# Kernel tuning notes

Hardware: AMD Instinct MI355X
Metric: run time of the kernel (lower is better)

## Reference

```python
import jax, jax.numpy as jnp
import numpy as np

HEADS = 8
DIM_HEAD = 64
IMG_SIZE = 32
KERNEL = 5
DILATION = 1
SEQ_LEN = 1280
IMG_SEQ_LEN = IMG_SIZE * IMG_SIZE  # 1024
TEXT_LEN = SEQ_LEN - IMG_SEQ_LEN   # 256


def _unfold(t, k, pad, dil, pad_value=0.0):
    # t: (b, c, H, W) -> (b, c, H*W, k*k), matching torch F.unfold ordering (c major)
    b, c, H, W = t.shape
    tp = jnp.pad(t, ((0, 0), (0, 0), (pad, pad), (pad, pad)), constant_values=pad_value)
    off = jnp.arange(k) * dil
    ys = jnp.arange(H)[:, None] + off[None, :]  # (H, k)
    xs = jnp.arange(W)[:, None] + off[None, :]  # (W, k)
    p = tp[:, :, ys[:, None, :, None], xs[None, :, None, :]]  # (b, c, H, W, k, k)
    return p.reshape(b, c, H * W, k * k)


def setup_inputs() -> dict:
    key = jax.random.key(0)
    k0, k1, k2 = jax.random.split(key, 3)
    b, n, dim = 4, SEQ_LEN, 512
    inner = HEADS * DIM_HEAD
    x = jax.random.normal(k0, (b, n, dim), dtype=jnp.float32)
    mask = jnp.ones((b, TEXT_LEN), dtype=bool)
    W_qkv = jax.random.normal(k1, (dim, 3 * inner), dtype=jnp.float32) * 0.02
    W_out = jax.random.normal(k2, (inner, dim), dtype=jnp.float32) * 0.02
    b_out = jnp.zeros((dim,), dtype=jnp.float32)
    return {"x": x, "mask": mask, "W_qkv": W_qkv, "W_out": W_out, "b_out": b_out}


def reference(x, mask, W_qkv, W_out, b_out):
    # t2i branch of SparseConvCausalAttention.forward
    b, n, dim = x.shape
    h, d = HEADS, DIM_HEAD
    scale = d ** -0.5
    neg = -jnp.finfo(x.dtype).max
    eff_k = (KERNEL - 1) * DILATION + 1
    pad = eff_k // 2

    qkv = x @ W_qkv  # (b, n, 3*h*d); n == SEQ_LEN so F.pad is a no-op
    qkv = qkv.reshape(b, n, 3, h, d).transpose(2, 0, 3, 1, 4).reshape(3, b * h, n, d)
    q, k, v = qkv[0] * scale, qkv[1], qkv[2]

    q_text, q_img = q[:, :TEXT_LEN], q[:, TEXT_LEN:]
    k_text, k_img = k[:, :TEXT_LEN], k[:, TEXT_LEN:]
    v_text, v_img = v[:, :TEXT_LEN], v[:, TEXT_LEN:]

    # --- text -> text causal attention ---
    dots_text = jnp.einsum('bid,bjd->bij', q_text, k_text)  # (bh, T, T)
    causal_t = jnp.triu(jnp.ones((TEXT_LEN, TEXT_LEN), bool), 1)
    pad_mask = jnp.repeat(mask, h, axis=0)[:, None, :]  # (bh, 1, T)
    dots_text = jnp.where(causal_t[None], neg, dots_text)
    dots_text = jnp.where(~pad_mask, neg, dots_text)
    attn_text = jax.nn.softmax(dots_text, axis=-1)
    out_text = jnp.einsum('bij,bjd->bid', attn_text, v_text)

    # --- image local-window (unfold) keys/values ---
    k_im = k_img.transpose(0, 2, 1).reshape(b * h, d, IMG_SIZE, IMG_SIZE)
    v_im = v_img.transpose(0, 2, 1).reshape(b * h, d, IMG_SIZE, IMG_SIZE)
    kk = KERNEL * KERNEL
    k_patch = _unfold(k_im, KERNEL, pad, DILATION).transpose(0, 2, 3, 1)  # (bh, I, kk, d)
    v_patch = _unfold(v_im, KERNEL, pad, DILATION).transpose(0, 2, 3, 1)

    dots_image = jnp.einsum('bid,bijd->bij', q_img, k_patch)       # (bh, I, kk)
    dots_i2t = jnp.einsum('bid,bjd->bij', q_img, k_text)           # (bh, I, T)

    # local causal mask via unfolded position indices (out-of-bounds -> IMG_SEQ_LEN)
    idx_img = jnp.arange(IMG_SEQ_LEN, dtype=jnp.float32).reshape(1, 1, IMG_SIZE, IMG_SIZE)
    k_idx = _unfold(idx_img, KERNEL, pad, DILATION, pad_value=float(IMG_SEQ_LEN))
    k_idx = k_idx.reshape(IMG_SEQ_LEN, kk)  # (I, kk)
    q_idx = jnp.arange(IMG_SEQ_LEN, dtype=jnp.float32)[:, None]
    causal_img = q_idx < k_idx  # (I, kk)

    full_mask = jnp.concatenate(
        (jnp.broadcast_to(~pad_mask, (b * h, IMG_SEQ_LEN, TEXT_LEN)),
         jnp.broadcast_to(causal_img[None], (b * h, IMG_SEQ_LEN, kk))), axis=-1)
    dots = jnp.concatenate((dots_i2t, dots_image), axis=-1)
    dots = jnp.where(full_mask, neg, dots)
    attn = jax.nn.softmax(dots, axis=-1)
    attn_i2t, attn_ii = attn[..., :TEXT_LEN], attn[..., TEXT_LEN:]

    out_img = (jnp.einsum('bij,bijd->bid', attn_ii, v_patch)
               + jnp.einsum('bij,bjd->bid', attn_i2t, v_text))

    out = jnp.concatenate((out_text, out_img), axis=1)  # (bh, n, d)
    out = out.reshape(b, h, n, d).transpose(0, 2, 1, 3).reshape(b, n, h * d)
    out = out @ W_out + b_out
    return out[:, :n]
```

## Files before the change

### kernel.cpp

```cpp
#include <hip/hip_runtime.h>
#include <math.h>

#define BATCH   4
#define NSEQ    1280
#define DIM     512
#define HEADS   8
#define DHEAD   64
#define TEXTLEN 256
#define IMGLEN  1024
#define BH      (BATCH*HEADS)

typedef __bf16 bf16x8 __attribute__((ext_vector_type(8)));
typedef float  f32x4  __attribute__((ext_vector_type(4)));
typedef unsigned short u16x4 __attribute__((ext_vector_type(4)));
typedef unsigned short u16x8 __attribute__((ext_vector_type(8)));

__device__ __forceinline__ unsigned short f2bf(float f) {
  unsigned int u = __float_as_uint(f);
  u += 0x7FFFu + ((u >> 16) & 1u);
  return (unsigned short)(u >> 16);
}

template<int MODE>
__global__ __launch_bounds__(256)
void mfma_gemm(const unsigned short* __restrict__ A,
               const unsigned short* __restrict__ BT,
               unsigned short* __restrict__ qb, unsigned short* __restrict__ kb,
               unsigned short* __restrict__ vb, unsigned short* __restrict__ vt,
               float* __restrict__ outb, const float* __restrict__ bias) {
  __shared__ __align__(16) unsigned short As[128*64];
  __shared__ __align__(16) unsigned short Bs[128*64];
  const int tid  = threadIdx.x;
  const int lane = tid & 63, w = tid >> 6;
  const int wm = w >> 1, wn = w & 1;
  const int lr = lane & 15, lg = lane >> 4;
  const int bx = blockIdx.x, by = blockIdx.y;

  f32x4 acc[4][4] = {};

  for (int kt = 0; kt < 512; kt += 64) {
    __syncthreads();
#pragma unroll
    for (int u = 0; u < 4; ++u) {
      const int idx = tid + u*256;
      const int row = idx >> 3, pq = idx & 7;
      const int sc  = ((pq ^ (row & 7)) << 3);
      const unsigned short* ga = A  + (size_t)(by*128 + row)*512 + kt + sc;
      const unsigned short* gb = BT + (size_t)(bx*128 + row)*512 + kt + sc;
      unsigned short* la = As + (((u << 8) + (w << 6)) << 3);
      unsigned short* lb = Bs + (((u << 8) + (w << 6)) << 3);
      __builtin_amdgcn_global_load_lds(
          (const __attribute__((address_space(1))) void*)ga,
          (__attribute__((address_space(3))) void*)la, 16, 0, 0);
      __builtin_amdgcn_global_load_lds(
          (const __attribute__((address_space(1))) void*)gb,
          (__attribute__((address_space(3))) void*)lb, 16, 0, 0);
    }
    __syncthreads();

#pragma unroll
    for (int kk = 0; kk < 2; ++kk) {
      bf16x8 af[4], bfr[4];
#pragma unroll
      for (int mi = 0; mi < 4; ++mi) {
        const int row = wm*64 + mi*16 + lr;
        const int q   = kk*4 + lg;
        af[mi] = *(const bf16x8*)&As[row*64 + ((q ^ (row & 7)) << 3)];
      }
#pragma unroll
      for (int ni = 0; ni < 4; ++ni) {
        const int n = wn*64 + ni*16 + lr;
        const int q = kk*4 + lg;
        bfr[ni] = *(const bf16x8*)&Bs[n*64 + ((q ^ (n & 7)) << 3)];
      }
#pragma unroll
      for (int mi = 0; mi < 4; ++mi)
#pragma unroll
        for (int ni = 0; ni < 4; ++ni)
          acc[mi][ni] = __builtin_amdgcn_mfma_f32_16x16x32_bf16(
              af[mi], bfr[ni], acc[mi][ni], 0, 0, 0);
    }
  }

  if (MODE == 0) {
    const int t  = bx >> 2, bxl = bx & 3;
    const int hh = bxl*2 + wn;
    const int bb = by / 10;
    const int nb = (by - bb*10) * 128;
    const float s = (t == 0) ? 0.125f : 1.0f;
    const size_t bh64 = (size_t)(bb*HEADS + hh);
    if (t != 2) {
      unsigned short* dst = (t == 0) ? qb : kb;
      unsigned short* base = dst + (bh64*NSEQ + nb)*DHEAD;
#pragma unroll
      for (int mi = 0; mi < 4; ++mi)
#pragma unroll
        for (int ni = 0; ni < 4; ++ni)
#pragma unroll
          for (int r = 0; r < 4; ++r) {
            const int rl = wm*64 + mi*16 + lg*4 + r;
            base[(size_t)rl*DHEAD + ni*16 + lr] = f2bf(acc[mi][ni][r] * s);
          }
    } else if (nb < 256) {
      unsigned short* vtb = vt + bh64*64*TEXTLEN;
#pragma unroll
      for (int mi = 0; mi < 4; ++mi)
#pragma unroll
        for (int ni = 0; ni < 4; ++ni)
#pragma unroll
          for (int r = 0; r < 4; ++r) {
            const int rl = wm*64 + mi*16 + lg*4 + r;
            const int d  = ni*16 + lr;
            vtb[(size_t)d*TEXTLEN + nb + rl] = f2bf(acc[mi][ni][r]);
          }
    } else {
      unsigned short* base = vb + (bh64*NSEQ + nb)*DHEAD;
#pragma unroll
      for (int mi = 0; mi < 4; ++mi)
#pragma unroll
        for (int ni = 0; ni < 4; ++ni)
#pragma unroll
          for (int r = 0; r < 4; ++r) {
            const int rl = wm*64 + mi*16 + lg*4 + r;
            base[(size_t)rl*DHEAD + ni*16 + lr] = f2bf(acc[mi][ni][r]);
          }
    }
  } else {
#pragma unroll
    for (int mi = 0; mi < 4; ++mi)
#pragma unroll
      for (int ni = 0; ni < 4; ++ni)
#pragma unroll
        for (int r = 0; r < 4; ++r) {
          const int gr = by*128 + wm*64 + mi*16 + lg*4 + r;
          const int gc = bx*128 + wn*64 + ni*16 + lr;
          outb[(size_t)gr*DIM + gc] = acc[mi][ni][r] + bias[gc];
        }
  }
}

__global__ __launch_bounds__(256)
void convert_bf16(const float* __restrict__ in, unsigned short* __restrict__ out,
                  int n) {
  const int i = (blockIdx.x*256 + threadIdx.x)*8;
  if (i < n) {
    const float4 a = *(const float4*)(in + i);
    const float4 b = *(const float4*)(in + i + 4);
    u16x8 pk;
    pk[0]=f2bf(a.x); pk[1]=f2bf(a.y); pk[2]=f2bf(a.z); pk[3]=f2bf(a.w);
    pk[4]=f2bf(b.x); pk[5]=f2bf(b.y); pk[6]=f2bf(b.z); pk[7]=f2bf(b.w);
    *(u16x8*)(out + i) = pk;
  }
}

__global__ __launch_bounds__(256)
void transpose_bf16(const float* __restrict__ in, unsigned short* __restrict__ out,
                    int K, int N) {
  __shared__ float t[64][65];
  const int k0 = blockIdx.y*64, n0 = blockIdx.x*64;
  const int tx = threadIdx.x & 15, ty = threadIdx.x >> 4;
#pragma unroll
  for (int rr = 0; rr < 4; ++rr) {
    const int k = ty + rr*16;
    const float4 v = *(const float4*)(in + (size_t)(k0 + k)*N + n0 + tx*4);
    t[k][tx*4+0] = v.x; t[k][tx*4+1] = v.y; t[k][tx*4+2] = v.z; t[k][tx*4+3] = v.w;
  }
  __syncthreads();
#pragma unroll
  for (int rr = 0; rr < 4; ++rr) {
    const int n = ty + rr*16;
    u16x4 pk;
#pragma unroll
    for (int j = 0; j < 4; ++j) pk[j] = f2bf(t[tx*4+j][n]);
    *(u16x4*)(out + (size_t)(n0 + n)*K + k0 + tx*4) = pk;
  }
}

__global__ __launch_bounds__(256)
void attn_qk(const unsigned short* __restrict__ qv,
             const unsigned short* __restrict__ kv,
             unsigned short* __restrict__ Pm, float* __restrict__ lpart) {
  __shared__ __align__(16) unsigned short As[128*64];
  __shared__ __align__(16) unsigned short Bs[128*64];
  const int tid  = threadIdx.x;
  const int lane = tid & 63, w = tid >> 6;
  const int wm = w >> 1, wn = w & 1;
  const int lr = lane & 15, lg = lane >> 4;
  const int bx = blockIdx.x, by = blockIdx.y;
  const int bh = by / 10, qt = by - bh*10;
  const bool textq = qt >= 8;
  const int qsrc  = textq ? (qt - 8)*128 : (TEXTLEN + qt*128);
  const int prow0 = qt*128;
  const int qg0   = (qt - 8)*128;

  {
    const unsigned short* ga0 = qv + ((size_t)bh*NSEQ + qsrc)*DHEAD;
    const unsigned short* gb0 = kv + ((size_t)bh*NSEQ + bx*128)*DHEAD;
#pragma unroll
    for (int u = 0; u < 4; ++u) {
      const int idx = tid + u*256;
      const int row = idx >> 3, pq = idx & 7;
      const int sc  = ((pq ^ (row & 7)) << 3);
      unsigned short* la = As + (((u << 8) + (w << 6)) << 3);
      unsigned short* lb = Bs + (((u << 8) + (w << 6)) << 3);
      __builtin_amdgcn_global_load_lds(
          (const __attribute__((address_space(1))) void*)(ga0 + (size_t)row*DHEAD + sc),
          (__attribute__((address_space(3))) void*)la, 16, 0, 0);
      __builtin_amdgcn_global_load_lds(
          (const __attribute__((address_space(1))) void*)(gb0 + (size_t)row*DHEAD + sc),
          (__attribute__((address_space(3))) void*)lb, 16, 0, 0);
    }
  }
  __syncthreads();

  f32x4 acc[4][4] = {};
#pragma unroll
  for (int kk = 0; kk < 2; ++kk) {
    bf16x8 af[4], bfr[4];
#pragma unroll
    for (int mi = 0; mi < 4; ++mi) {
      const int row = wm*64 + mi*16 + lr;
      const int q   = kk*4 + lg;
      af[mi] = *(const bf16x8*)&As[row*64 + ((q ^ (row & 7)) << 3)];
    }
#pragma unroll
    for (int ni = 0; ni < 4; ++ni) {
      const int n = wn*64 + ni*16 + lr;
      const int q = kk*4 + lg;
      bfr[ni] = *(const bf16x8*)&Bs[n*64 + ((q ^ (n & 7)) << 3)];
    }
#pragma unroll
    for (int mi = 0; mi < 4; ++mi)
#pragma unroll
      for (int ni = 0; ni < 4; ++ni)
        acc[mi][ni] = __builtin_amdgcn_mfma_f32_16x16x32_bf16(
            af[mi], bfr[ni], acc[mi][ni], 0, 0, 0);
  }

  unsigned short* pbase = Pm + ((size_t)bh*NSEQ + prow0)*TEXTLEN;
  float* lbase = lpart + ((size_t)bh*NSEQ + prow0)*4;
#pragma unroll
  for (int mi = 0; mi < 4; ++mi)
#pragma unroll
    for (int r = 0; r < 4; ++r) {
      const int q_local = wm*64 + mi*16 + lg*4 + r;
      float ps = 0.f;
#pragma unroll
      for (int ni = 0; ni < 4; ++ni) {
        const int key = bx*128 + wn*64 + ni*16 + lr;
        float wv = __expf(acc[mi][ni][r]);
        if (textq && key > qg0 + q_local) wv = 0.f;
        ps += wv;
        pbase[(size_t)q_local*TEXTLEN + key] = f2bf(wv);
      }
      ps += __shfl_xor(ps, 1);
      ps += __shfl_xor(ps, 2);
      ps += __shfl_xor(ps, 4);
      ps += __shfl_xor(ps, 8);
      if (lr == 0) lbase[(size_t)q_local*4 + bx*2 + wn] = ps;
    }
}

__global__ __launch_bounds__(256)
void attn_pv(const unsigned short* __restrict__ Pm,
             const unsigned short* __restrict__ vt,
             float* __restrict__ Of) {
  __shared__ __align__(16) unsigned short As[256*64];
  __shared__ __align__(16) unsigned short Bs[64*64];
  const int tid  = threadIdx.x;
  const int lane = tid & 63, w = tid >> 6;
  const int lr = lane & 15, lg = lane >> 4;
  const int mt = blockIdx.x, bh = blockIdx.y;

  f32x4 acc[4][4] = {};

  for (int kt = 0; kt < TEXTLEN; kt += 64) {
    __syncthreads();
    {
      const unsigned short* ga0 = Pm + ((size_t)bh*NSEQ + mt*256)*TEXTLEN + kt;
      const unsigned short* gb0 = vt + ((size_t)bh*DHEAD)*TEXTLEN + kt;
#pragma unroll
      for (int u = 0; u < 8; ++u) {
        const int idx = tid + u*256;
        const int row = idx >> 3, pq = idx & 7;
        const int sc  = ((pq ^ (row & 7)) << 3);
        unsigned short* la = As + (((u << 8) + (w << 6)) << 3);
        __builtin_amdgcn_global_load_lds(
            (const __attribute__((address_space(1))) void*)(ga0 + (size_t)row*TEXTLEN + sc),
            (__attribute__((address_space(3))) void*)la, 16, 0, 0);
      }
#pragma unroll
      for (int u = 0; u < 2; ++u) {
        const int idx = tid + u*256;
        const int row = idx >> 3, pq = idx & 7;
        const int sc  = ((pq ^ (row & 7)) << 3);
        unsigned short* lb = Bs + (((u << 8) + (w << 6)) << 3);
        __builtin_amdgcn_global_load_lds(
            (const __attribute__((address_space(1))) void*)(gb0 + (size_t)row*TEXTLEN + sc),
            (__attribute__((address_space(3))) void*)lb, 16, 0, 0);
      }
    }
    __syncthreads();

#pragma unroll
    for (int kk = 0; kk < 2; ++kk) {
      bf16x8 af[4], bfr[4];
#pragma unroll
      for (int mi = 0; mi < 4; ++mi) {
        const int row = w*64 + mi*16 + lr;
        const int q   = kk*4 + lg;
        af[mi] = *(const bf16x8*)&As[row*64 + ((q ^ (row & 7)) << 3)];
      }
#pragma unroll
      for (int ni = 0; ni < 4; ++ni) {
        const int n = ni*16 + lr;
        const int q = kk*4 + lg;
        bfr[ni] = *(const bf16x8*)&Bs[n*64 + ((q ^ (n & 7)) << 3)];
      }
#pragma unroll
      for (int mi = 0; mi < 4; ++mi)
#pragma unroll
        for (int ni = 0; ni < 4; ++ni)
          acc[mi][ni] = __builtin_amdgcn_mfma_f32_16x16x32_bf16(
              af[mi], bfr[ni], acc[mi][ni], 0, 0, 0);
    }
  }

  float* obase = Of + ((size_t)bh*NSEQ + mt*256)*DHEAD;
#pragma unroll
  for (int mi = 0; mi < 4; ++mi)
#pragma unroll
    for (int ni = 0; ni < 4; ++ni)
#pragma unroll
      for (int r = 0; r < 4; ++r) {
        const int row = w*64 + mi*16 + lg*4 + r;
        obase[(size_t)row*DHEAD + ni*16 + lr] = acc[mi][ni][r];
      }
}

__global__ __launch_bounds__(256)
void attn_fin(const unsigned short* __restrict__ qv,
              const unsigned short* __restrict__ kv,
              const unsigned short* __restrict__ vb,
              const float* __restrict__ Of, const float* __restrict__ lpart,
              unsigned short* __restrict__ ab) {
  const int blk = blockIdx.x;
  const int bh = blk / 40, sub = blk - bh*40;
  const int bb = bh >> 3, hh = bh & 7;
  const int gq = threadIdx.x >> 3;
  const int s8 = threadIdx.x & 7;
  const int prow = sub*32 + gq;
  const bool img = prow < IMGLEN;
  const int qrow = img ? (TEXTLEN + prow) : (prow - IMGLEN);

  float o[8];
  {
    const float4 a = *(const float4*)(Of + ((size_t)bh*NSEQ + prow)*DHEAD + s8*8);
    const float4 b = *(const float4*)(Of + ((size_t)bh*NSEQ + prow)*DHEAD + s8*8 + 4);
    o[0]=a.x; o[1]=a.y; o[2]=a.z; o[3]=a.w; o[4]=b.x; o[5]=b.y; o[6]=b.z; o[7]=b.w;
  }
  float l;
  {
    const float4 lp = *(const float4*)(lpart + ((size_t)bh*NSEQ + prow)*4);
    l = lp.x + lp.y + lp.z + lp.w;
  }

  if (img) {
    float qd[8];
    {
      const bf16x8 q8 = *(const bf16x8*)(qv + ((size_t)bh*NSEQ + qrow)*DHEAD + s8*8);
#pragma unroll
      for (int e = 0; e < 8; ++e) qd[e] = (float)q8[e];
    }
    const int yy = prow >> 5, xx = prow & 31;
    for (int nb = 0; nb < 13; ++nb) {
      const int q5 = nb / 5;
      const int ny = yy + q5 - 2;
      const int nx = xx + (nb - q5*5) - 2;
      const bool ok = (ny >= 0) && ((unsigned)nx < 32u);
      const int kidx = ok ? (ny*32 + nx) : prow;
      const bf16x8 k8 = *(const bf16x8*)(kv + ((size_t)bh*NSEQ + TEXTLEN + kidx)*DHEAD + s8*8);
      float d = 0.f;
#pragma unroll
      for (int e = 0; e < 8; ++e) d += qd[e]*(float)k8[e];
      d += __shfl_xor(d, 1);
      d += __shfl_xor(d, 2);
      d += __shfl_xor(d, 4);
      const float wv = ok ? __expf(d) : 0.f;
      l += wv;
      const bf16x8 v8 = *(const bf16x8*)(vb + ((size_t)bh*NSEQ + TEXTLEN + kidx)*DHEAD + s8*8);
#pragma unroll
      for (int e = 0; e < 8; ++e) o[e] += wv*(float)v8[e];
    }
  }

  const float inv = 1.f / l;
  u16x8 pk;
#pragma unroll
  for (int e = 0; e < 8; ++e) pk[e] = f2bf(o[e]*inv);
  *(u16x8*)(ab + ((size_t)(bb*NSEQ) + qrow)*DIM + hh*DHEAD + s8*8) = pk;
}

extern "C" void kernel_launch(void* const* d_in, const int* in_sizes, int n_in,
                              void* d_out, int out_size, void* d_ws, size_t ws_size,
                              hipStream_t stream) {
  const float* x     = (const float*)d_in[0];
  const float* W_qkv = (const float*)d_in[2];
  const float* W_out = (const float*)d_in[3];
  const float* b_out = (const float*)d_in[4];
  float* out = (float*)d_out;

  unsigned short* w = (unsigned short*)d_ws;
  const size_t P = (size_t)BH*NSEQ*DHEAD;
  unsigned short* qb  = w;
  unsigned short* kb  = qb + P;
  unsigned short* vb  = kb + P;
  unsigned short* xb  = vb + P;
  unsigned short* ab  = xb;
  unsigned short* wtq = xb + P;
  unsigned short* wto = wtq + (size_t)1536*512;
  unsigned short* vtb = wto + (size_t)512*512;
  unsigned short* Pm  = vtb + (size_t)BH*DHEAD*TEXTLEN;
  float* Of    = (float*)(Pm + (size_t)BH*NSEQ*TEXTLEN);
  float* lpart = Of + (size_t)BH*NSEQ*DHEAD;

  convert_bf16<<<(BATCH*NSEQ*DIM)/(256*8), 256, 0, stream>>>(x, xb, BATCH*NSEQ*DIM);
  transpose_bf16<<<dim3(24, 8), 256, 0, stream>>>(W_qkv, wtq, 512, 1536);
  transpose_bf16<<<dim3(8, 8), 256, 0, stream>>>(W_out, wto, 512, 512);

  mfma_gemm<0><<<dim3(12, 40), 256, 0, stream>>>(
      xb, wtq, qb, kb, vb, vtb, nullptr, nullptr);

  attn_qk<<<dim3(2, 320), 256, 0, stream>>>(qb, kb, Pm, lpart);
  attn_pv<<<dim3(5, 32), 256, 0, stream>>>(Pm, vtb, Of);
  attn_fin<<<1280, 256, 0, stream>>>(qb, kb, vb, Of, lpart, ab);

  mfma_gemm<1><<<dim3(4, 40), 256, 0, stream>>>(
      ab, wto, nullptr, nullptr, nullptr, nullptr, out, b_out);
}
```

Baseline: 76.02 us.

## Fuse text QK and PV attention kernels and merge prep kernels

Merges the x conversion and both weight transposes into a single prep launch that dispatches on block index. Replaces the separate attn_qk and attn_pv kernels with one attn_qkpv kernel. Each block loads all 256 text keys plus its 128 queries, writes the exp scores and partial row sums, then reloads the transposed V into the same shared buffer and computes P·V for its rows. This removes two kernel launches and the separate PV pass's re-staging of P through shared memory. In exchange the fused kernel uses more accumulator registers and runs fewer blocks, and it reads P back from global memory right after writing it.

```diff
diff --git a/kernel.cpp b/kernel.cpp
--- a/kernel.cpp
+++ b/kernel.cpp
@@ -140,24 +140,28 @@
 }
 
 __global__ __launch_bounds__(256)
-void convert_bf16(const float* __restrict__ in, unsigned short* __restrict__ out,
-                  int n) {
-  const int i = (blockIdx.x*256 + threadIdx.x)*8;
-  if (i < n) {
-    const float4 a = *(const float4*)(in + i);
-    const float4 b = *(const float4*)(in + i + 4);
+void prep(const float* __restrict__ x, unsigned short* __restrict__ xb,
+          const float* __restrict__ Wq, unsigned short* __restrict__ wtq,
+          const float* __restrict__ Wo, unsigned short* __restrict__ wto) {
+  __shared__ float t[64][65];
+  const int b = blockIdx.x;
+  if (b < 1280) {
+    const int i = (b*256 + threadIdx.x)*8;
+    const float4 a = *(const float4*)(x + i);
+    const float4 c = *(const float4*)(x + i + 4);
     u16x8 pk;
     pk[0]=f2bf(a.x); pk[1]=f2bf(a.y); pk[2]=f2bf(a.z); pk[3]=f2bf(a.w);
-    pk[4]=f2bf(b.x); pk[5]=f2bf(b.y); pk[6]=f2bf(b.z); pk[7]=f2bf(b.w);
-    *(u16x8*)(out + i) = pk;
-  }
-}
-
-__global__ __launch_bounds__(256)
-void transpose_bf16(const float* __restrict__ in, unsigned short* __restrict__ out,
-                    int K, int N) {
-  __shared__ float t[64][65];
-  const int k0 = blockIdx.y*64, n0 = blockIdx.x*64;
+    pk[4]=f2bf(c.x); pk[5]=f2bf(c.y); pk[6]=f2bf(c.z); pk[7]=f2bf(c.w);
+    *(u16x8*)(xb + i) = pk;
+    return;
+  }
+  const bool isq = b < 1472;
+  const int bi  = isq ? (b - 1280) : (b - 1472);
+  const int nt  = isq ? 24 : 8;
+  const int N   = isq ? 1536 : 512;
+  const float* in = isq ? Wq : Wo;
+  unsigned short* out = isq ? wtq : wto;
+  const int n0 = (bi % nt)*64, k0 = (bi / nt)*64;
   const int tx = threadIdx.x & 15, ty = threadIdx.x >> 4;
 #pragma unroll
   for (int rr = 0; rr < 4; ++rr) {
@@ -172,21 +176,23 @@
     u16x4 pk;
 #pragma unroll
     for (int j = 0; j < 4; ++j) pk[j] = f2bf(t[tx*4+j][n]);
-    *(u16x4*)(out + (size_t)(n0 + n)*K + k0 + tx*4) = pk;
+    *(u16x4*)(out + (size_t)(n0 + n)*512 + k0 + tx*4) = pk;
   }
 }
 
 __global__ __launch_bounds__(256)
-void attn_qk(const unsigned short* __restrict__ qv,
-             const unsigned short* __restrict__ kv,
-             unsigned short* __restrict__ Pm, float* __restrict__ lpart) {
-  __shared__ __align__(16) unsigned short As[128*64];
-  __shared__ __align__(16) unsigned short Bs[128*64];
+void attn_qkpv(const unsigned short* __restrict__ qv,
+               const unsigned short* __restrict__ kv,
+               const unsigned short* __restrict__ vt,
+               unsigned short* __restrict__ Pm,
+               float* __restrict__ Of, float* __restrict__ lpart) {
+  __shared__ __align__(16) unsigned short Ks[256*64];
+  __shared__ __align__(16) unsigned short Qs[128*64];
   const int tid  = threadIdx.x;
   const int lane = tid & 63, w = tid >> 6;
   const int wm = w >> 1, wn = w & 1;
   const int lr = lane & 15, lg = lane >> 4;
-  const int bx = blockIdx.x, by = blockIdx.y;
+  const int by = blockIdx.x;
   const int bh = by / 10, qt = by - bh*10;
   const bool textq = qt >= 8;
   const int qsrc  = textq ? (qt - 8)*128 : (TEXTLEN + qt*128);
@@ -194,147 +200,133 @@
   const int qg0   = (qt - 8)*128;
 
   {
-    const unsigned short* ga0 = qv + ((size_t)bh*NSEQ + qsrc)*DHEAD;
-    const unsigned short* gb0 = kv + ((size_t)bh*NSEQ + bx*128)*DHEAD;
+    const unsigned short* kg = kv + (size_t)bh*NSEQ*DHEAD;
+    const unsigned short* qg = qv + ((size_t)bh*NSEQ + qsrc)*DHEAD;
+#pragma unroll
+    for (int u = 0; u < 8; ++u) {
+      const int ci = tid + u*256;
+      const int row = ci >> 3, cq = ci & 7;
+      const unsigned short* gsrc = kg + (size_t)row*DHEAD + ((cq ^ (row & 7)) << 3);
+      unsigned short* ldst = Ks + (((u << 8) + (w << 6)) << 3);
+      __builtin_amdgcn_global_load_lds(
+          (const __attribute__((address_space(1))) void*)gsrc,
+          (__attribute__((address_space(3))) void*)ldst, 16, 0, 0);
+    }
 #pragma unroll
     for (int u = 0; u < 4; ++u) {
-      const int idx = tid + u*256;
-      const int row = idx >> 3, pq = idx & 7;
-      const int sc  = ((pq ^ (row & 7)) << 3);
-      unsigned short* la = As + (((u << 8) + (w << 6)) << 3);
-      unsigned short* lb = Bs + (((u << 8) + (w << 6)) << 3);
+      const int ci = tid + u*256;
+      const int row = ci >> 3, cq = ci & 7;
+      const unsigned short* gsrc = qg + (size_t)row*DHEAD + ((cq ^ (row & 7)) << 3);
+      unsigned short* ldst = Qs + (((u << 8) + (w << 6)) << 3);
       __builtin_amdgcn_global_load_lds(
-          (const __attribute__((address_space(1))) void*)(ga0 + (size_t)row*DHEAD + sc),
-          (__attribute__((address_space(3))) void*)la, 16, 0, 0);
-      __builtin_amdgcn_global_load_lds(
-          (const __attribute__((address_space(1))) void*)(gb0 + (size_t)row*DHEAD + sc),
-          (__attribute__((address_space(3))) void*)lb, 16, 0, 0);
+          (const __attribute__((address_space(1))) void*)gsrc,
+          (__attribute__((address_space(3))) void*)ldst, 16, 0, 0);
     }
   }
   __syncthreads();
 
-  f32x4 acc[4][4] = {};
+  f32x4 acc[4][8] = {};
 #pragma unroll
   for (int kk = 0; kk < 2; ++kk) {
-    bf16x8 af[4], bfr[4];
+    bf16x8 af[4], bfr[8];
 #pragma unroll
     for (int mi = 0; mi < 4; ++mi) {
       const int row = wm*64 + mi*16 + lr;
       const int q   = kk*4 + lg;
-      af[mi] = *(const bf16x8*)&As[row*64 + ((q ^ (row & 7)) << 3)];
-    }
-#pragma unroll
-    for (int ni = 0; ni < 4; ++ni) {
-      const int n = wn*64 + ni*16 + lr;
+      af[mi] = *(const bf16x8*)&Qs[row*64 + ((q ^ (row & 7)) << 3)];
+    }
+#pragma unroll
+    for (int ni = 0; ni < 8; ++ni) {
+      const int n = wn*128 + ni*16 + lr;
       const int q = kk*4 + lg;
-      bfr[ni] = *(const bf16x8*)&Bs[n*64 + ((q ^ (n & 7)) << 3)];
+      bfr[ni] = *(const bf16x8*)&Ks[n*64 + ((q ^ (n & 7)) << 3)];
     }
 #pragma unroll
     for (int mi = 0; mi < 4; ++mi)
 #pragma unroll
-      for (int ni = 0; ni < 4; ++ni)
+      for (int ni = 0; ni < 8; ++ni)
         acc[mi][ni] = __builtin_amdgcn_mfma_f32_16x16x32_bf16(
             af[mi], bfr[ni], acc[mi][ni], 0, 0, 0);
   }
 
-  unsigned short* pbase = Pm + ((size_t)bh*NSEQ + prow0)*TEXTLEN;
-  float* lbase = lpart + ((size_t)bh*NSEQ + prow0)*4;
-#pragma unroll
-  for (int mi = 0; mi < 4; ++mi)
-#pragma unroll
-    for (int r = 0; r < 4; ++r) {
-      const int q_local = wm*64 + mi*16 + lg*4 + r;
-      float ps = 0.f;
+  {
+    unsigned short* pbase = Pm + ((size_t)bh*NSEQ + prow0)*TEXTLEN;
+    float* lbase = lpart + ((size_t)bh*NSEQ + prow0)*2;
+#pragma unroll
+    for (int mi = 0; mi < 4; ++mi)
+#pragma unroll
+      for (int r = 0; r < 4; ++r) {
+        const int row = wm*64 + mi*16 + lg*4 + r;
+        float ps = 0.f;
+#pragma unroll
+        for (int ni = 0; ni < 8; ++ni) {
+          const int key = wn*128 + ni*16 + lr;
+          const float wv = (textq && key > qg0 + row) ? 0.f
+                                                      : __expf(acc[mi][ni][r]);
+          ps += wv;
+          pbase[(size_t)row*TEXTLEN + key] = f2bf(wv);
+        }
+        ps += __shfl_xor(ps, 1);
+        ps += __shfl_xor(ps, 2);
+        ps += __shfl_xor(ps, 4);
+        ps += __shfl_xor(ps, 8);
+        if (lr == 0) lbase[(size_t)row*2 + wn] = ps;
+      }
+  }
+
+  __syncthreads();
+
+  {
+    const unsigned short* vtg = vt + (size_t)bh*DHEAD*TEXTLEN;
+#pragma unroll
+    for (int u = 0; u < 8; ++u) {
+      const int ci = tid + u*256;
+      const int row = ci >> 5, cq = ci & 31;
+      const unsigned short* gsrc = vtg + (size_t)row*TEXTLEN + ((cq ^ (row & 7)) << 3);
+      unsigned short* ldst = Ks + (((u << 8) + (w << 6)) << 3);
+      __builtin_amdgcn_global_load_lds(
+          (const __attribute__((address_space(1))) void*)gsrc,
+          (__attribute__((address_space(3))) void*)ldst, 16, 0, 0);
+    }
+  }
+  __syncthreads();
+
+  f32x4 acc2[2][4] = {};
+  const unsigned short* prb = Pm + ((size_t)bh*NSEQ + prow0)*TEXTLEN;
+#pragma unroll
+  for (int kt = 0; kt < TEXTLEN; kt += 64) {
+#pragma unroll
+    for (int kk = 0; kk < 2; ++kk) {
+      bf16x8 paf[2], vbf[4];
+#pragma unroll
+      for (int mi = 0; mi < 2; ++mi) {
+        const int row = w*32 + mi*16 + lr;
+        paf[mi] = *(const bf16x8*)(prb + (size_t)row*TEXTLEN + kt + ((kk*4 + lg) << 3));
+      }
 #pragma unroll
       for (int ni = 0; ni < 4; ++ni) {
-        const int key = bx*128 + wn*64 + ni*16 + lr;
-        float wv = __expf(acc[mi][ni][r]);
-        if (textq && key > qg0 + q_local) wv = 0.f;
-        ps += wv;
-        pbase[(size_t)q_local*TEXTLEN + key] = f2bf(wv);
-      }
-      ps += __shfl_xor(ps, 1);
-      ps += __shfl_xor(ps, 2);
-      ps += __shfl_xor(ps, 4);
-      ps += __shfl_xor(ps, 8);
-      if (lr == 0) lbase[(size_t)q_local*4 + bx*2 + wn] = ps;
-    }
-}
-
-__global__ __launch_bounds__(256)
-void attn_pv(const unsigned short* __restrict__ Pm,
-             const unsigned short* __restrict__ vt,
-             float* __restrict__ Of) {
-  __shared__ __align__(16) unsigned short As[256*64];
-  __shared__ __align__(16) unsigned short Bs[64*64];
-  const int tid  = threadIdx.x;
-  const int lane = tid & 63, w = tid >> 6;
-  const int lr = lane & 15, lg = lane >> 4;
-  const int mt = blockIdx.x, bh = blockIdx.y;
-
-  f32x4 acc[4][4] = {};
-
-  for (int kt = 0; kt < TEXTLEN; kt += 64) {
-    __syncthreads();
-    {
-      const unsigned short* ga0 = Pm + ((size_t)bh*NSEQ + mt*256)*TEXTLEN + kt;
-      const unsigned short* gb0 = vt + ((size_t)bh*DHEAD)*TEXTLEN + kt;
-#pragma unroll
-      for (int u = 0; u < 8; ++u) {
-        const int idx = tid + u*256;
-        const int row = idx >> 3, pq = idx & 7;
-        const int sc  = ((pq ^ (row & 7)) << 3);
-        unsigned short* la = As + (((u << 8) + (w << 6)) << 3);
-        __builtin_amdgcn_global_load_lds(
-            (const __attribute__((address_space(1))) void*)(ga0 + (size_t)row*TEXTLEN + sc),
-            (__attribute__((address_space(3))) void*)la, 16, 0, 0);
-      }
-#pragma unroll
-      for (int u = 0; u < 2; ++u) {
-        const int idx = tid + u*256;
-        const int row = idx >> 3, pq = idx & 7;
-        const int sc  = ((pq ^ (row & 7)) << 3);
-        unsigned short* lb = Bs + (((u << 8) + (w << 6)) << 3);
-        __builtin_amdgcn_global_load_lds(
-            (const __attribute__((address_space(1))) void*)(gb0 + (size_t)row*TEXTLEN + sc),
-            (__attribute__((address_space(3))) void*)lb, 16, 0, 0);
-      }
-    }
-    __syncthreads();
-
-#pragma unroll
-    for (int kk = 0; kk < 2; ++kk) {
-      bf16x8 af[4], bfr[4];
-#pragma unroll
-      for (int mi = 0; mi < 4; ++mi) {
-        const int row = w*64 + mi*16 + lr;
-        const int q   = kk*4 + lg;
-        af[mi] = *(const bf16x8*)&As[row*64 + ((q ^ (row & 7)) << 3)];
-      }
-#pragma unroll
-      for (int ni = 0; ni < 4; ++ni) {
-        const int n = ni*16 + lr;
-        const int q = kk*4 + lg;
-        bfr[ni] = *(const bf16x8*)&Bs[n*64 + ((q ^ (n & 7)) << 3)];
-      }
-#pragma unroll
-      for (int mi = 0; mi < 4; ++mi)
+        const int d = ni*16 + lr;
+        const int chunk = (kt >> 3) + kk*4 + lg;
+        vbf[ni] = *(const bf16x8*)&Ks[d*256 + ((chunk ^ (d & 7)) << 3)];
+      }
+#pragma unroll
+      for (int mi = 0; mi < 2; ++mi)
 #pragma unroll
         for (int ni = 0; ni < 4; ++ni)
-          acc[mi][ni] = __builtin_amdgcn_mfma_f32_16x16x32_bf16(
-              af[mi], bfr[ni], acc[mi][ni], 0, 0, 0);
-    }
-  }
-
-  float* obase = Of + ((size_t)bh*NSEQ + mt*256)*DHEAD;
-#pragma unroll
-  for (int mi = 0; mi < 4; ++mi)
+          acc2[mi][ni] = __builtin_amdgcn_mfma_f32_16x16x32_bf16(
+              paf[mi], vbf[ni], acc2[mi][ni], 0, 0, 0);
+    }
+  }
+
+  float* obase = Of + ((size_t)bh*NSEQ + prow0)*DHEAD;
+#pragma unroll
+  for (int mi = 0; mi < 2; ++mi)
 #pragma unroll
     for (int ni = 0; ni < 4; ++ni)
 #pragma unroll
       for (int r = 0; r < 4; ++r) {
-        const int row = w*64 + mi*16 + lg*4 + r;
-        obase[(size_t)row*DHEAD + ni*16 + lr] = acc[mi][ni][r];
+        const int row = w*32 + mi*16 + lg*4 + r;
+        obase[(size_t)row*DHEAD + ni*16 + lr] = acc2[mi][ni][r];
       }
 }
 
@@ -361,8 +353,8 @@
   }
   float l;
   {
-    const float4 lp = *(const float4*)(lpart + ((size_t)bh*NSEQ + prow)*4);
-    l = lp.x + lp.y + lp.z + lp.w;
+    const float2 lp = *(const float2*)(lpart + ((size_t)bh*NSEQ + prow)*2);
+    l = lp.x + lp.y;
   }
 
   if (img) {
@@ -424,15 +416,12 @@
   float* Of    = (float*)(Pm + (size_t)BH*NSEQ*TEXTLEN);
   float* lpart = Of + (size_t)BH*NSEQ*DHEAD;
 
-  convert_bf16<<<(BATCH*NSEQ*DIM)/(256*8), 256, 0, stream>>>(x, xb, BATCH*NSEQ*DIM);
-  transpose_bf16<<<dim3(24, 8), 256, 0, stream>>>(W_qkv, wtq, 512, 1536);
-  transpose_bf16<<<dim3(8, 8), 256, 0, stream>>>(W_out, wto, 512, 512);
+  prep<<<1536, 256, 0, stream>>>(x, xb, W_qkv, wtq, W_out, wto);
 
   mfma_gemm<0><<<dim3(12, 40), 256, 0, stream>>>(
       xb, wtq, qb, kb, vb, vtb, nullptr, nullptr);
 
-  attn_qk<<<dim3(2, 320), 256, 0, stream>>>(qb, kb, Pm, lpart);
-  attn_pv<<<dim3(5, 32), 256, 0, stream>>>(Pm, vtb, Of);
+  attn_qkpv<<<320, 256, 0, stream>>>(qb, kb, vtb, Pm, Of, lpart);
   attn_fin<<<1280, 256, 0, stream>>>(qb, kb, vb, Of, lpart, ab);
 
   mfma_gemm<1><<<dim3(4, 40), 256, 0, stream>>>(
```

Measured after the change: 76.63 us. No clear change (+0.8%).
